# Kernel tuning notes

Measured on AMD Instinct MI355X. Metric: run time of the kernel, lower is better.

## Reference

```python
import jax, jax.numpy as jnp
import numpy as np

B, N, K, D = 256, 64, 12, 128


def setup_inputs() -> dict:
    key = jax.random.key(0)
    ks = jax.random.split(key, 12)
    s = 1.0 / np.sqrt(D)
    inp = {
        "nodes_hidden": jax.random.normal(ks[0], (B, N, D), jnp.float32),
        "neighbors_hidden": jax.random.normal(ks[1], (B, N, K, D), jnp.float32),
        # binary neighbor-validity mask (float, as in the torch code)
        "mask": (jax.random.uniform(ks[2], (B, N, K)) < 0.7).astype(jnp.float32),
        "Wq": jax.random.uniform(ks[3], (D, D), jnp.float32, -s, s),
        "bq": jax.random.uniform(ks[4], (D,), jnp.float32, -s, s),
        "Wk": jax.random.uniform(ks[5], (D, D), jnp.float32, -s, s),
        "bk": jax.random.uniform(ks[6], (D,), jnp.float32, -s, s),
        "Wv": jax.random.uniform(ks[7], (D, D), jnp.float32, -s, s),
        "bv": jax.random.uniform(ks[8], (D,), jnp.float32, -s, s),
        # W_att: Linear(2D -> 1); split into the query half and key half of its weight
        "wa_q": jax.random.uniform(ks[9], (D,), jnp.float32, -s, s),
        "wa_k": jax.random.uniform(ks[10], (D,), jnp.float32, -s, s),
        "ba": jax.random.uniform(ks[11], (), jnp.float32, -s, s),
    }
    return inp


def reference(nodes_hidden, neighbors_hidden, mask, Wq, bq, Wk, bk, Wv, bv, wa_q, wa_k, ba):
    # prepend the node itself to its neighbor list: [B,N,K+1,D]
    nh = jnp.concatenate([nodes_hidden[:, :, None, :], neighbors_hidden], axis=2)
    # prepend an always-valid slot to the mask: [B,N,K+1]
    m = jnp.concatenate([jnp.ones(mask.shape[:-1] + (1,), mask.dtype), mask], axis=-1)

    q = nodes_hidden @ Wq + bq            # [B,N,D]
    k = nh @ Wk + bk                      # [B,N,K+1,D]
    v = nh @ Wv + bv                      # [B,N,K+1,D]

    # W_att(cat([q,k])) == q.wa_q + k.wa_k + ba  (avoids materializing the 2D concat)
    sim = (q @ wa_q)[:, :, None] + k @ wa_k + ba   # [B,N,K+1]
    sim = jnp.where(sim >= 0, sim, 0.2 * sim)      # LeakyReLU(0.2)
    sim = jnp.exp(sim) * m                         # masked exp (matches torch exactly)
    attn = sim / (jnp.sum(sim, axis=-1, keepdims=True) + 1e-16)
    return jnp.einsum('bnk,bnkd->bnd', attn, v)    # [B,N,D]
```

## Files before the change

### kernel.cpp

```cpp
#include <hip/hip_runtime.h>


#define B_  256
#define N_  64
#define K_  12
#define D_  128
#define BN  (B_ * N_)
#define ROWS 16
#define NBLK (BN / ROWS)
#define HB_STRIDE 132

__global__ void __launch_bounds__(256, 4)
fused_kernel(const float* __restrict__ nodes, const float* __restrict__ neigh,
             const float* __restrict__ mask,
             const float* __restrict__ Wq, const float* __restrict__ bq,
             const float* __restrict__ Wk, const float* __restrict__ bk,
             const float* __restrict__ Wv, const float* __restrict__ bv,
             const float* __restrict__ wa_q, const float* __restrict__ wa_k,
             const float* __restrict__ ba_p, float* __restrict__ out) {
    __shared__ float weff[256];
    __shared__ float hb[ROWS * HB_STRIDE];
    __shared__ float scL[ROWS];
    __shared__ float cstS;

    const int t    = threadIdx.x;
    const int wave = t >> 6;
    const int l    = t & 63;

    {
        const bool  isQ  = (wave < 2);
        const float* Wm  = isQ ? Wq : Wk;
        const float* wav = isQ ? wa_q : wa_k;
        const int sub    = l & 15;
        const int rquad  = l >> 4;
        const int rbase  = (wave & 1) * 64;
        const int obase  = isQ ? 0 : 128;
        float4 wv0 = ((const float4*)wav)[sub * 2];
        float4 wv1 = ((const float4*)wav)[sub * 2 + 1];
        #pragma unroll 4
        for (int i = 0; i < 16; ++i) {
            int r = rbase + i * 4 + rquad;
            const float4* wr = (const float4*)(Wm + (size_t)r * D_);
            float4 a0 = wr[sub * 2], a1 = wr[sub * 2 + 1];
            float p = a0.x * wv0.x + a0.y * wv0.y + a0.z * wv0.z + a0.w * wv0.w
                    + a1.x * wv1.x + a1.y * wv1.y + a1.z * wv1.z + a1.w * wv1.w;
            p += __shfl_xor(p, 1, 64);
            p += __shfl_xor(p, 2, 64);
            p += __shfl_xor(p, 4, 64);
            p += __shfl_xor(p, 8, 64);
            if (sub == 0) weff[obase + r] = p;
        }
    }
    if (wave == 0) {
        float2 q2  = ((const float2*)bq)[l];
        float2 k2  = ((const float2*)bk)[l];
        float2 aq2 = ((const float2*)wa_q)[l];
        float2 ak2 = ((const float2*)wa_k)[l];
        float c = q2.x * aq2.x + q2.y * aq2.y + k2.x * ak2.x + k2.y * ak2.y;
        #pragma unroll
        for (int m = 1; m < 64; m <<= 1) c += __shfl_xor(c, m, 64);
        if (l == 0) cstS = c + ba_p[0];
    }
    __syncthreads();

    const float cst = cstS;
    const int h = l >> 5;
    const int s = l & 31;
    const float4 wqe = ((const float4*)weff)[s];
    const float4 wke = ((const float4*)(weff + 128))[s];

    #pragma unroll
    for (int i = 0; i < 2; ++i) {
        const int lrow = wave * 4 + i * 2 + h;
        const int idx  = blockIdx.x * ROWS + lrow;

        const float4* np = (const float4*)(nodes + (size_t)idx * D_);
        const float4* gp = (const float4*)(neigh + (size_t)idx * (K_ * D_));

        float4 x[K_ + 1];
        x[0] = np[s];
        #pragma unroll
        for (int j = 0; j < K_; ++j) x[j + 1] = gp[j * 32 + s];

        float mval = (s < K_) ? mask[(size_t)idx * K_ + s] : 0.0f;
        unsigned long long mbits = __ballot(mval > 0.5f);

        float pq = x[0].x * wqe.x + x[0].y * wqe.y + x[0].z * wqe.z + x[0].w * wqe.w;
        float tj[K_ + 1];
        #pragma unroll
        for (int j = 0; j <= K_; ++j)
            tj[j] = pq + x[j].x * wke.x + x[j].y * wke.y
                       + x[j].z * wke.z + x[j].w * wke.w;

        #pragma unroll
        for (int m = 1; m < 32; m <<= 1) {
            #pragma unroll
            for (int j = 0; j <= K_; ++j) tj[j] += __shfl_xor(tj[j], m, 64);
        }

        float e[K_ + 1];
        float S = 0.0f;
        #pragma unroll
        for (int j = 0; j <= K_; ++j) {
            float sc = tj[j] + cst;
            sc = (sc >= 0.0f) ? sc : 0.2f * sc;
            float mj = (j == 0) ? 1.0f
                     : (((mbits >> (h * 32 + j - 1)) & 1ull) ? 1.0f : 0.0f);
            e[j] = __expf(sc) * mj;
            S += e[j];
        }
        const float inv = 1.0f / (S + 1e-16f);

        float4 hacc = make_float4(0.f, 0.f, 0.f, 0.f);
        #pragma unroll
        for (int j = 0; j <= K_; ++j) {
            float w = e[j] * inv;
            hacc.x += w * x[j].x;  hacc.y += w * x[j].y;
            hacc.z += w * x[j].z;  hacc.w += w * x[j].w;
        }
        *(float4*)(hb + lrow * HB_STRIDE + s * 4) = hacc;
        if (s == 0) scL[lrow] = S * inv;
    }
    __syncthreads();

    const int rg   = t >> 5;
    const int cg   = t & 31;
    const int row0 = blockIdx.x * ROWS;
    const float4* wv4 = (const float4*)Wv;

    float4 acc0 = make_float4(0.f, 0.f, 0.f, 0.f);
    float4 acc1 = make_float4(0.f, 0.f, 0.f, 0.f);
    #pragma unroll 4
    for (int k4 = 0; k4 < 32; ++k4) {
        float4 a0 = *(const float4*)(hb + rg * HB_STRIDE + k4 * 4);
        float4 a1 = *(const float4*)(hb + (rg + 8) * HB_STRIDE + k4 * 4);
        #pragma unroll
        for (int kk = 0; kk < 4; ++kk) {
            float4 b  = wv4[(k4 * 4 + kk) * 32 + cg];
            float av0 = (&a0.x)[kk];
            float av1 = (&a1.x)[kk];
            acc0.x += av0 * b.x;  acc0.y += av0 * b.y;
            acc0.z += av0 * b.z;  acc0.w += av0 * b.w;
            acc1.x += av1 * b.x;  acc1.y += av1 * b.y;
            acc1.z += av1 * b.z;  acc1.w += av1 * b.w;
        }
    }

    float4 bvv = ((const float4*)bv)[cg];
    {
        float sc = scL[rg];
        float4 o;
        o.x = acc0.x + bvv.x * sc;  o.y = acc0.y + bvv.y * sc;
        o.z = acc0.z + bvv.z * sc;  o.w = acc0.w + bvv.w * sc;
        *(float4*)(out + (size_t)(row0 + rg) * D_ + cg * 4) = o;
    }
    {
        float sc = scL[rg + 8];
        float4 o;
        o.x = acc1.x + bvv.x * sc;  o.y = acc1.y + bvv.y * sc;
        o.z = acc1.z + bvv.z * sc;  o.w = acc1.w + bvv.w * sc;
        *(float4*)(out + (size_t)(row0 + rg + 8) * D_ + cg * 4) = o;
    }
}

extern "C" void kernel_launch(void* const* d_in, const int* in_sizes, int n_in,
                              void* d_out, int out_size, void* d_ws, size_t ws_size,
                              hipStream_t stream) {
    const float* nodes = (const float*)d_in[0];
    const float* neigh = (const float*)d_in[1];
    const float* mask  = (const float*)d_in[2];
    const float* Wq    = (const float*)d_in[3];
    const float* bq    = (const float*)d_in[4];
    const float* Wk    = (const float*)d_in[5];
    const float* bk    = (const float*)d_in[6];
    const float* Wv    = (const float*)d_in[7];
    const float* bv    = (const float*)d_in[8];
    const float* wa_q  = (const float*)d_in[9];
    const float* wa_k  = (const float*)d_in[10];
    const float* ba    = (const float*)d_in[11];
    float* out = (float*)d_out;

    fused_kernel<<<NBLK, 256, 0, stream>>>(nodes, neigh, mask, Wq, bq, Wk, bk,
                                           Wv, bv, wa_q, wa_k, ba, out);
}
```

Baseline: 203.5 us.

## Stage neighbor rows in shared memory as fp16 and halve rows per block

Neighbor vectors are no longer held in registers across the score reduction. They are converted to half precision, parked in shared memory, and read back for the weighted sum, which cuts register pressure. Rows per block drop from 16 to 8, so each thread handles one row and the grid doubles. The cost is that the per-block weight-effective precompute and the Wv matrix read repeat twice as often, and the aggregation loses some precision from fp16 rounding.

```diff
diff --git a/kernel.cpp b/kernel.cpp
--- a/kernel.cpp
+++ b/kernel.cpp
@@ -1,4 +1,5 @@
 #include <hip/hip_runtime.h>
+#include <hip/hip_fp16.h>
 
 
 #define B_  256
@@ -6,9 +7,11 @@
 #define K_  12
 #define D_  128
 #define BN  (B_ * N_)
-#define ROWS 16
+#define ROWS 8
 #define NBLK (BN / ROWS)
 #define HB_STRIDE 132
+
+struct h4 { __half2 lo, hi; };
 
 __global__ void __launch_bounds__(256, 4)
 fused_kernel(const float* __restrict__ nodes, const float* __restrict__ neigh,
@@ -19,6 +22,7 @@
              const float* __restrict__ wa_q, const float* __restrict__ wa_k,
              const float* __restrict__ ba_p, float* __restrict__ out) {
     __shared__ float weff[256];
+    __shared__ h4    stg[4][2][K_][32];
     __shared__ float hb[ROWS * HB_STRIDE];
     __shared__ float scL[ROWS];
     __shared__ float cstS;
@@ -69,28 +73,33 @@
     const float4 wqe = ((const float4*)weff)[s];
     const float4 wke = ((const float4*)(weff + 128))[s];
 
-    #pragma unroll
-    for (int i = 0; i < 2; ++i) {
-        const int lrow = wave * 4 + i * 2 + h;
+    {
+        const int lrow = wave * 2 + h;
         const int idx  = blockIdx.x * ROWS + lrow;
 
         const float4* np = (const float4*)(nodes + (size_t)idx * D_);
         const float4* gp = (const float4*)(neigh + (size_t)idx * (K_ * D_));
 
-        float4 x[K_ + 1];
-        x[0] = np[s];
+        float4 x0 = np[s];
+        float pq = x0.x * wqe.x + x0.y * wqe.y + x0.z * wqe.z + x0.w * wqe.w;
+
+        float tj[K_ + 1];
+        tj[0] = pq + x0.x * wke.x + x0.y * wke.y + x0.z * wke.z + x0.w * wke.w;
+
+        h4* sp = &stg[wave][h][0][s];
         #pragma unroll
-        for (int j = 0; j < K_; ++j) x[j + 1] = gp[j * 32 + s];
+        for (int j = 0; j < K_; ++j) {
+            float4 xj = gp[j * 32 + s];
+            tj[j + 1] = pq + xj.x * wke.x + xj.y * wke.y
+                           + xj.z * wke.z + xj.w * wke.w;
+            h4 p;
+            p.lo = __floats2half2_rn(xj.x, xj.y);
+            p.hi = __floats2half2_rn(xj.z, xj.w);
+            sp[j * 32] = p;
+        }
 
         float mval = (s < K_) ? mask[(size_t)idx * K_ + s] : 0.0f;
         unsigned long long mbits = __ballot(mval > 0.5f);
-
-        float pq = x[0].x * wqe.x + x[0].y * wqe.y + x[0].z * wqe.z + x[0].w * wqe.w;
-        float tj[K_ + 1];
-        #pragma unroll
-        for (int j = 0; j <= K_; ++j)
-            tj[j] = pq + x[j].x * wke.x + x[j].y * wke.y
-                       + x[j].z * wke.z + x[j].w * wke.w;
 
         #pragma unroll
         for (int m = 1; m < 32; m <<= 1) {
@@ -111,12 +120,18 @@
         }
         const float inv = 1.0f / (S + 1e-16f);
 
-        float4 hacc = make_float4(0.f, 0.f, 0.f, 0.f);
+        float w0 = e[0] * inv;
+        float4 hacc;
+        hacc.x = w0 * x0.x;  hacc.y = w0 * x0.y;
+        hacc.z = w0 * x0.z;  hacc.w = w0 * x0.w;
         #pragma unroll
-        for (int j = 0; j <= K_; ++j) {
-            float w = e[j] * inv;
-            hacc.x += w * x[j].x;  hacc.y += w * x[j].y;
-            hacc.z += w * x[j].z;  hacc.w += w * x[j].w;
+        for (int j = 0; j < K_; ++j) {
+            h4 p = sp[j * 32];
+            float2 a = __half22float2(p.lo);
+            float2 b = __half22float2(p.hi);
+            float w = e[j + 1] * inv;
+            hacc.x += w * a.x;  hacc.y += w * a.y;
+            hacc.z += w * b.x;  hacc.w += w * b.y;
         }
         *(float4*)(hb + lrow * HB_STRIDE + s * 4) = hacc;
         if (s == 0) scL[lrow] = S * inv;
@@ -128,39 +143,21 @@
     const int row0 = blockIdx.x * ROWS;
     const float4* wv4 = (const float4*)Wv;
 
-    float4 acc0 = make_float4(0.f, 0.f, 0.f, 0.f);
-    float4 acc1 = make_float4(0.f, 0.f, 0.f, 0.f);
-    #pragma unroll 4
-    for (int k4 = 0; k4 < 32; ++k4) {
-        float4 a0 = *(const float4*)(hb + rg * HB_STRIDE + k4 * 4);
-        float4 a1 = *(const float4*)(hb + (rg + 8) * HB_STRIDE + k4 * 4);
-        #pragma unroll
-        for (int kk = 0; kk < 4; ++kk) {
-            float4 b  = wv4[(k4 * 4 + kk) * 32 + cg];
-            float av0 = (&a0.x)[kk];
-            float av1 = (&a1.x)[kk];
-            acc0.x += av0 * b.x;  acc0.y += av0 * b.y;
-            acc0.z += av0 * b.z;  acc0.w += av0 * b.w;
-            acc1.x += av1 * b.x;  acc1.y += av1 * b.y;
-            acc1.z += av1 * b.z;  acc1.w += av1 * b.w;
-        }
+    float4 acc = make_float4(0.f, 0.f, 0.f, 0.f);
+    #pragma unroll 8
+    for (int k = 0; k < D_; ++k) {
+        float4 b = wv4[k * 32 + cg];
+        float  a = hb[rg * HB_STRIDE + k];
+        acc.x += a * b.x;  acc.y += a * b.y;
+        acc.z += a * b.z;  acc.w += a * b.w;
     }
 
     float4 bvv = ((const float4*)bv)[cg];
-    {
-        float sc = scL[rg];
-        float4 o;
-        o.x = acc0.x + bvv.x * sc;  o.y = acc0.y + bvv.y * sc;
-        o.z = acc0.z + bvv.z * sc;  o.w = acc0.w + bvv.w * sc;
-        *(float4*)(out + (size_t)(row0 + rg) * D_ + cg * 4) = o;
-    }
-    {
-        float sc = scL[rg + 8];
-        float4 o;
-        o.x = acc1.x + bvv.x * sc;  o.y = acc1.y + bvv.y * sc;
-        o.z = acc1.z + bvv.z * sc;  o.w = acc1.w + bvv.w * sc;
-        *(float4*)(out + (size_t)(row0 + rg + 8) * D_ + cg * 4) = o;
-    }
+    float  sc  = scL[rg];
+    float4 o;
+    o.x = acc.x + bvv.x * sc;  o.y = acc.y + bvv.y * sc;
+    o.z = acc.z + bvv.z * sc;  o.w = acc.w + bvv.w * sc;
+    *(float4*)(out + (size_t)(row0 + rg) * D_ + cg * 4) = o;
 }
 
 extern "C" void kernel_launch(void* const* d_in, const int* in_sizes, int n_in,
```

Result: slower. 212.6 us (+4.5%).
